# Kernel tuning notes

Measured on AMD Instinct MI355X. Metric: run time of the kernel, lower is better.

The kernel has to match this reference:

```python
import jax, jax.numpy as jnp
import numpy as np

NV, NG, D, K, NB = 4096, 2048, 64, 128, 4
C_IN, C_OUT, E = 128, 8, 32768
SIGMA = 2.5  # rbf sigma used in the non-mp path


def _gcn_conv(x, src, dst, w, b, n):
    # PyG GCNConv (edge_weight=None, self loops already appended to src/dst)
    deg = jax.ops.segment_sum(jnp.ones(src.shape, x.dtype), dst, num_segments=n)
    dinv = jnp.where(deg > 0, 1.0 / jnp.sqrt(deg), 0.0)
    norm = dinv[src] * dinv[dst]
    h = x @ w
    return jax.ops.segment_sum(h[src] * norm[:, None], dst, num_segments=n) + b


def _diff_block(x, mass, evals, evecs, gradX, gradY, t, a_re, a_im, w0, b0, w1, b1, w2, b2):
    # learned-time spectral diffusion
    x_spec = evecs.T @ (x * mass[:, None])                      # [K, D]
    coef = jnp.exp(-evals[:, None] * jnp.clip(t, 1e-8)[None, :])  # [K, D]
    x_diff = evecs @ (coef * x_spec)                            # [NV, D]
    # spatial gradient features: complex grad, learned rotation, tanh of inner product
    gX = gradX @ x_diff                                         # real part  [NV, D]
    gY = gradY @ x_diff                                         # imag part  [NV, D]
    b_re = gX @ a_re - gY @ a_im
    b_im = gY @ a_re + gX @ a_im
    gfeat = jnp.tanh(gX * b_re + gY * b_im)
    f = jnp.concatenate([x, x_diff, gfeat], axis=-1)            # [NV, 3D]
    h = jax.nn.relu(f @ w0 + b0)
    h = jax.nn.relu(h @ w1 + b1)
    return h @ w2 + b2 + x                                      # residual skip


def _forward(surf_x, mass, evals, evecs, gradX, gradY, vertices, graph_x, graph_pos,
             lin1_w, lin1_b, lin2_w, lin2_b, last_w, last_b,
             diff_time, A_re, A_im, mlp_w0, mlp_b0, mlp_w1, mlp_b1, mlp_w2, mlp_b2,
             gcn_w1, gcn_b1, gcn_w2, gcn_b2, edge_index):
    nv, ng = vertices.shape[0], graph_pos.shape[0]
    # dense rbf coupling (torch.no_grad in original -> stop_gradient)
    d2 = (jnp.sum(vertices * vertices, 1)[:, None]
          + jnp.sum(graph_pos * graph_pos, 1)[None, :]
          - 2.0 * (vertices @ graph_pos.T))
    dist = jnp.sqrt(jnp.clip(d2, 0.0))
    rbf = jax.lax.stop_gradient(jnp.exp(-dist / SIGMA))          # [NV, NG]
    diff_x = surf_x @ lin1_w + lin1_b                            # [NV, D]
    gx = graph_x @ lin2_w + lin2_b                               # [NG, D]
    loops = jnp.arange(ng, dtype=edge_index.dtype)
    src = jnp.concatenate([edge_index[0], loops])
    dst = jnp.concatenate([edge_index[1], loops])
    for i in range(NB):
        diff_x = _diff_block(diff_x, mass, evals, evecs, gradX, gradY,
                             diff_time[i], A_re[i], A_im[i],
                             mlp_w0[i], mlp_b0[i], mlp_w1[i], mlp_b1[i], mlp_w2[i], mlp_b2[i])
        gx = rbf.T @ diff_x                                      # surface -> graph
        h = jax.nn.relu(_gcn_conv(gx, src, dst, gcn_w1[i], gcn_b1[i], ng))
        gx = _gcn_conv(h, src, dst, gcn_w2[i], gcn_b2[i], ng)
        diff_x = rbf @ gx                                        # graph -> surface
    return diff_x @ last_w + last_b                              # [NV, C_OUT]


def setup_inputs() -> dict:
    key = jax.random.key(0)
    ks = jax.random.split(key, 24)
    f32 = jnp.float32
    def rn(k, shape, scale=1.0):
        return jax.random.normal(k, shape, f32) * scale
    inp = {
        'surf_x': rn(ks[0], (NV, 5)),
        'mass': jax.random.uniform(ks[1], (NV,), f32, 0.1, 1.0),
        'evals': jnp.sort(jax.random.uniform(ks[2], (K,), f32, 0.0, 50.0)),
        'evecs': rn(ks[3], (NV, K), 1.0 / np.sqrt(NV)),
        'gradX': rn(ks[4], (NV, NV), 1.0 / np.sqrt(NV)),
        'gradY': rn(ks[5], (NV, NV), 1.0 / np.sqrt(NV)),
        'vertices': rn(ks[6], (NV, 3), 5.0),
        'graph_x': rn(ks[7], (NG, C_IN)),
        'graph_pos': rn(ks[8], (NG, 3), 5.0),
        'lin1_w': rn(ks[9], (5, D), 1.0 / np.sqrt(5)),
        'lin1_b': jnp.zeros((D,), f32),
        'lin2_w': rn(ks[10], (C_IN, D), 1.0 / np.sqrt(C_IN)),
        'lin2_b': jnp.zeros((D,), f32),
        'last_w': rn(ks[11], (D, C_OUT), 1.0 / np.sqrt(D)),
        'last_b': jnp.zeros((C_OUT,), f32),
        'diff_time': jax.random.uniform(ks[12], (NB, D), f32, 1e-3, 1.0),
        'A_re': rn(ks[13], (NB, D, D), 1.0 / np.sqrt(D)),
        'A_im': rn(ks[14], (NB, D, D), 1.0 / np.sqrt(D)),
        'mlp_w0': rn(ks[15], (NB, 3 * D, D), 1.0 / np.sqrt(3 * D)),
        'mlp_b0': jnp.zeros((NB, D), f32),
        'mlp_w1': rn(ks[16], (NB, D, D), 1.0 / np.sqrt(D)),
        'mlp_b1': jnp.zeros((NB, D), f32),
        'mlp_w2': rn(ks[17], (NB, D, D), 1.0 / np.sqrt(D)),
        'mlp_b2': jnp.zeros((NB, D), f32),
        'gcn_w1': rn(ks[18], (NB, D, D), 1.0 / np.sqrt(D)),
        'gcn_b1': jnp.zeros((NB, D), f32),
        'gcn_w2': rn(ks[19], (NB, D, D), 1.0 / np.sqrt(D)),
        'gcn_b2': jnp.zeros((NB, D), f32),
        'edge_index': jax.random.randint(ks[20], (2, E), 0, NG, dtype=jnp.int32),
    }
    return inp


def reference(surf_x, mass, evals, evecs, gradX, gradY, vertices, graph_x, graph_pos,
              lin1_w, lin1_b, lin2_w, lin2_b, last_w, last_b,
              diff_time, A_re, A_im, mlp_w0, mlp_b0, mlp_w1, mlp_b1, mlp_w2, mlp_b2,
              gcn_w1, gcn_b1, gcn_w2, gcn_b2, edge_index):
    return _forward(surf_x, mass, evals, evecs, gradX, gradY, vertices, graph_x, graph_pos,
                    lin1_w, lin1_b, lin2_w, lin2_b, last_w, last_b,
                    diff_time, A_re, A_im, mlp_w0, mlp_b0, mlp_w1, mlp_b1, mlp_w2, mlp_b2,
                    gcn_w1, gcn_b1, gcn_w2, gcn_b2, edge_index)
```

## Files before the change

kernel.cpp:

```cpp
#include <hip/hip_runtime.h>
#include <hip/hip_bf16.h>

#define NVV 4096
#define NGG 2048
#define DD 64
#define KSP 128
#define NBLK 4
#define NEDGE 32768
#define COUT 8
#define NSLICE_P 8
#define NSLICE_G 16
#define NSLICE_V 8
#define NSLICE_S 32
#define VS 32

typedef __hip_bfloat16 bf16;
using bf16x8 = __attribute__((ext_vector_type(8))) __bf16;
using s16x8  = __attribute__((ext_vector_type(8))) short;
using f32x4  = __attribute__((ext_vector_type(4))) float;

__device__ __forceinline__ float toF(bf16 x){ return __bfloat162float(x); }
__device__ __forceinline__ float ldin(const void* p, size_t i, int f){
  return f ? toF(((const bf16*)p)[i]) : ((const float*)p)[i];
}
__device__ __forceinline__ short f2bf(float x){
  __bf16 b = (__bf16)x;
  return __builtin_bit_cast(short, b);
}
__device__ __forceinline__ float bf2f(short s){
  return (float)__builtin_bit_cast(__bf16, s);
}
__device__ __forceinline__ bf16x8 ld8(const short* p){
  return __builtin_bit_cast(bf16x8, *(const s16x8*)p);
}
__device__ __forceinline__ void gl16(const short* g, short* l){
  __builtin_amdgcn_global_load_lds((__attribute__((address_space(1))) void*)(g),
                                   (__attribute__((address_space(3))) void*)(l),
                                   16, 0, 0);
}

__global__ void k_probe(const void* __restrict__ mass, int* __restrict__ flag){
  int t = threadIdx.x;
  float v = toF(((const bf16*)mass)[t]);
  bool ok = (v >= 0.05f) && (v <= 1.05f);
  unsigned long long m = __ballot(ok);
  if (t == 0) flag[0] = (m == ~0ull) ? 1 : 0;
}

__global__ void k_csr_zero(int* c){ int g = blockIdx.x*256+threadIdx.x; if (g<NGG) c[g]=0; }
__global__ void k_csr_cnt(const int* __restrict__ ei, int* __restrict__ c){
  int e = blockIdx.x*256+threadIdx.x; if (e<NEDGE) atomicAdd(&c[ei[NEDGE+e]], 1);
}
__global__ void k_csr_scan(const int* __restrict__ cnt, int* __restrict__ off,
                           int* __restrict__ cursor, float* __restrict__ dinv){
  __shared__ int ws[256];
  int t = threadIdx.x;
  int base = t*8;
  int local[8]; int s = 0;
  #pragma unroll
  for (int i=0;i<8;i++){ local[i]=s; s += cnt[base+i]; }
  ws[t] = s;
  __syncthreads();
  for (int o=1;o<256;o<<=1){
    int v = (t>=o) ? ws[t-o] : 0;
    __syncthreads();
    ws[t] += v;
    __syncthreads();
  }
  int pre = (t==0) ? 0 : ws[t-1];
  #pragma unroll
  for (int i=0;i<8;i++){
    int o = pre + local[i];
    off[base+i] = o; cursor[base+i] = o;
    dinv[base+i] = rsqrtf(1.f + (float)cnt[base+i]);
  }
  if (t==255) off[NGG] = pre + s;
}
__global__ void k_csr_fill(const int* __restrict__ ei, int* __restrict__ cursor,
                           int* __restrict__ csrc){
  int e = blockIdx.x*256+threadIdx.x;
  if (e < NEDGE){
    int d = ei[NEDGE+e];
    int p = atomicAdd(&cursor[d], 1);
    csrc[p] = ei[e];
  }
}

__global__ void k_lin1_mx(const void* __restrict__ sx, const void* __restrict__ w,
                          const void* __restrict__ b, const void* __restrict__ mass,
                          float* __restrict__ out, short* __restrict__ btMX,
                          const int* __restrict__ flg){
  const int f = *flg;
  __shared__ short tl[64*68];
  const int t = threadIdx.x;
  const int r = t>>2, c0 = (t&3)*16;
  const size_t v = (size_t)blockIdx.x*64 + r;
  float sxa[5];
  #pragma unroll
  for (int k=0;k<5;k++) sxa[k] = ldin(sx, v*5+k, f);
  const float mv = ldin(mass, v, f);
  float acc[16];
  #pragma unroll
  for (int j=0;j<16;j++){
    float a = ldin(b, c0+j, f);
    #pragma unroll
    for (int k=0;k<5;k++) a += sxa[k]*ldin(w, (size_t)k*DD + c0 + j, f);
    acc[j] = a;
    tl[(size_t)(c0+j)*68 + r] = f2bf(a*mv);
  }
  float* op = out + v*DD + c0;
  ((float4*)op)[0] = *(float4*)&acc[0];
  ((float4*)op)[1] = *(float4*)&acc[4];
  ((float4*)op)[2] = *(float4*)&acc[8];
  ((float4*)op)[3] = *(float4*)&acc[12];
  __syncthreads();
  s16x8 u0, u1;
  #pragma unroll
  for (int j=0;j<8;j++){ u0[j]=tl[(size_t)r*68+c0+j]; u1[j]=tl[(size_t)r*68+c0+8+j]; }
  const int s8 = (r&7)<<3;
  short* dp = btMX + (size_t)blockIdx.x*4096 + (size_t)r*64;
  *(s16x8*)&dp[c0 ^ s8]     = u0;
  *(s16x8*)&dp[(c0+8) ^ s8] = u1;
}

__global__ void k_spec_red(const float* __restrict__ partial, const void* __restrict__ evals,
                           const void* __restrict__ tvec, int boff,
                           short* __restrict__ btA, const int* __restrict__ flg){
  const int f = *flg;
  int idx = blockIdx.x*256 + threadIdx.x;
  int k = idx >> 6, d = idx & 63;
  float sum = 0.f;
  #pragma unroll 8
  for (int s = 0; s < VS; s++) sum += partial[(size_t)s*KSP*DD + idx];
  float t = fmaxf(ldin(tvec, boff + d, f), 1e-8f);
  float val = expf(-ldin(evals, k, f) * t) * sum;
  btA[(size_t)(k>>6)*4096 + (size_t)d*64 + ((k&63) ^ ((d&7)<<3))] = f2bf(val);
}

__global__ void k_cvt_a(const void* __restrict__ src, short* __restrict__ dst,
                        int Kfull, const int* __restrict__ flg){
  const int f = *flg;
  const int t = threadIdx.x;
  const int r = t>>2, c0 = (t&3)*16;
  const size_t row = (size_t)blockIdx.x*64 + r;
  const size_t base = row*(size_t)Kfull + (size_t)blockIdx.y*64 + c0;
  s16x8 v0, v1;
  if (f){
    const short* sp = (const short*)src + base;
    v0 = ((const s16x8*)sp)[0];
    v1 = ((const s16x8*)sp)[1];
  } else {
    const float* sp = (const float*)src + base;
    float tmp[16];
    ((float4*)tmp)[0] = ((const float4*)sp)[0];
    ((float4*)tmp)[1] = ((const float4*)sp)[1];
    ((float4*)tmp)[2] = ((const float4*)sp)[2];
    ((float4*)tmp)[3] = ((const float4*)sp)[3];
    #pragma unroll
    for (int i=0;i<8;i++){ v0[i]=f2bf(tmp[i]); v1[i]=f2bf(tmp[8+i]); }
  }
  const int s8 = (r&7)<<3;
  short* dp = dst + ((size_t)blockIdx.x*(Kfull>>6) + blockIdx.y)*4096 + (size_t)r*64;
  *(s16x8*)&dp[c0 ^ s8]     = v0;
  *(s16x8*)&dp[(c0+8) ^ s8] = v1;
}

__global__ void k_cvt_at(const void* __restrict__ evecs, short* __restrict__ dst,
                         const int* __restrict__ flg){
  const int f = *flg;
  __shared__ short tl[64*68];
  const int t = threadIdx.x;
  const int r = t>>2, c0 = (t&3)*16;
  const int kt = blockIdx.x, s = blockIdx.y;
  const size_t v = (size_t)kt*64 + r;
  #pragma unroll
  for (int j=0;j<16;j++)
    tl[(size_t)(c0+j)*68 + r] = f2bf(ldin(evecs, v*KSP + (size_t)s*64 + c0 + j, f));
  __syncthreads();
  s16x8 u0, u1;
  #pragma unroll
  for (int j=0;j<8;j++){ u0[j]=tl[(size_t)r*68+c0+j]; u1[j]=tl[(size_t)r*68+c0+8+j]; }
  const int s8 = (r&7)<<3;
  short* dp = dst + ((size_t)s*64 + kt)*4096 + (size_t)r*64;
  *(s16x8*)&dp[c0 ^ s8]     = u0;
  *(s16x8*)&dp[(c0+8) ^ s8] = u1;
}

__global__ void k_rbf_pre(const void* __restrict__ P, const void* __restrict__ Q,
                          short* __restrict__ rbfV, short* __restrict__ rbfG,
                          const int* __restrict__ flg){
  const int f = *flg;
  __shared__ short tl[64*68];
  const int t = threadIdx.x;
  const int r = t>>2, c0 = (t&3)*16;
  const int vt = blockIdx.x, gt = blockIdx.y;
  const float px = ldin(P, ((size_t)vt*64+r)*3+0, f);
  const float py = ldin(P, ((size_t)vt*64+r)*3+1, f);
  const float pz = ldin(P, ((size_t)vt*64+r)*3+2, f);
  s16x8 v0, v1;
  #pragma unroll
  for (int j=0;j<16;j++){
    const size_t g = (size_t)gt*64 + c0 + j;
    float dx = px - ldin(Q, g*3+0, f);
    float dy = py - ldin(Q, g*3+1, f);
    float dz = pz - ldin(Q, g*3+2, f);
    short s = f2bf(__expf(-sqrtf(dx*dx+dy*dy+dz*dz)*0.4f));
    if (j<8) v0[j] = s; else v1[j-8] = s;
    tl[(size_t)(c0+j)*68 + r] = s;
  }
  const int s8 = (r&7)<<3;
  short* vp = rbfV + ((size_t)vt*(NGG/64) + gt)*4096 + (size_t)r*64;
  *(s16x8*)&vp[c0 ^ s8]     = v0;
  *(s16x8*)&vp[(c0+8) ^ s8] = v1;
  __syncthreads();
  s16x8 u0, u1;
  #pragma unroll
  for (int j=0;j<8;j++){ u0[j] = tl[(size_t)r*68 + c0 + j]; u1[j] = tl[(size_t)r*68 + c0 + 8 + j]; }
  short* gp = rbfG + ((size_t)gt*(NVV/64) + vt)*4096 + (size_t)r*64;
  *(s16x8*)&gp[c0 ^ s8]     = u0;
  *(s16x8*)&gp[(c0+8) ^ s8] = u1;
}

__global__ void k_cvt_wt(const void* __restrict__ Are, const void* __restrict__ Aim,
                         const void* __restrict__ w0, const void* __restrict__ w1,
                         const void* __restrict__ w2,
                         short* __restrict__ btRe, short* __restrict__ btIm,
                         short* __restrict__ btW0, short* __restrict__ btW1,
                         short* __restrict__ btW2, const int* __restrict__ flg){
  const int f = *flg;
  __shared__ short tl[64*68];
  const int t = threadIdx.x;
  const int r = t>>2, c0 = (t&3)*16;
  const int slot = blockIdx.x, b = blockIdx.y;
  const void* src; size_t soff; short* dst; float scale = 1.f;
  switch(slot){
    case 0: src=Are; soff=(size_t)b*4096; dst=btRe + (size_t)b*2*4096;               break;
    case 1: src=Aim; soff=(size_t)b*4096; dst=btRe + (size_t)b*2*4096 + 4096; scale=-1.f; break;
    case 2: src=Aim; soff=(size_t)b*4096; dst=btIm + (size_t)b*2*4096;               break;
    case 3: src=Are; soff=(size_t)b*4096; dst=btIm + (size_t)b*2*4096 + 4096;        break;
    case 4: case 5: case 6:
      src=w0; soff=(size_t)b*3*4096 + (size_t)(slot-4)*4096;
      dst=btW0 + (size_t)b*3*4096 + (size_t)(slot-4)*4096;                           break;
    case 7: src=w1; soff=(size_t)b*4096; dst=btW1 + (size_t)b*4096;                  break;
    default: src=w2; soff=(size_t)b*4096; dst=btW2 + (size_t)b*4096;                 break;
  }
  #pragma unroll
  for (int j=0;j<16;j++)
    tl[(size_t)(c0+j)*68 + r] = f2bf(scale * ldin(src, soff + (size_t)r*64 + c0 + j, f));
  __syncthreads();
  s16x8 u0, u1;
  #pragma unroll
  for (int j=0;j<8;j++){ u0[j]=tl[(size_t)r*68+c0+j]; u1[j]=tl[(size_t)r*68+c0+8+j]; }
  const int s8 = (r&7)<<3;
  short* dp = dst + (size_t)r*64;
  *(s16x8*)&dp[c0 ^ s8]     = u0;
  *(s16x8*)&dp[(c0+8) ^ s8] = u1;
}

template<int TWO>
__global__ void k_gemm_pre(const short* __restrict__ A0, const short* __restrict__ A1,
                           const short* __restrict__ Bt, float* __restrict__ C,
                           int M, int ktt, int tps, int yoff, short* __restrict__ btOut){
  constexpr int NBUF = TWO ? 3 : 2;
  __shared__ __align__(16) short sm[2*NBUF*4096];
  const int t = threadIdx.x;
  const int w = t>>6, lane = t&63;
  const int fr = lane&15, fq = lane>>4;
  const int strip = blockIdx.x, sl = blockIdx.y;
  const size_t abase = ((size_t)strip*ktt + (size_t)sl*tps)*4096;
  const short* gA0 = A0 + abase;
  const short* gA1 = TWO ? (A1 + abase) : A0;
  const short* gB  = Bt + (size_t)sl*tps*4096;
  const int to = t*8;

  auto stage = [&](int p, int kt){
    short* l = &sm[p*NBUF*4096];
    const size_t ko = (size_t)kt*4096;
    gl16(gA0 + ko + to,        l + (w<<9));
    gl16(gA0 + ko + 2048 + to, l + 2048 + (w<<9));
    if (TWO){
      gl16(gA1 + ko + to,        l + 4096 + (w<<9));
      gl16(gA1 + ko + 2048 + to, l + 6144 + (w<<9));
    }
    short* lb = l + (TWO ? 8192 : 4096);
    gl16(gB + ko + to,        lb + (w<<9));
    gl16(gB + ko + 2048 + to, lb + 2048 + (w<<9));
  };

  f32x4 acc0[4] = {{0,0,0,0},{0,0,0,0},{0,0,0,0},{0,0,0,0}};
  f32x4 acc1[4] = {{0,0,0,0},{0,0,0,0},{0,0,0,0},{0,0,0,0}};

  stage(0, 0);
  int cur = 0;
  const int arow = w*16 + fr;
  const int ax0 = arow*64;
  const int asw = (arow&7)<<3;
  for (int kt=0; kt<tps; ++kt){
    if (kt+1 < tps){
      stage(cur^1, kt+1);
      if constexpr (TWO) asm volatile("s_waitcnt vmcnt(6)" ::: "memory");
      else               asm volatile("s_waitcnt vmcnt(4)" ::: "memory");
    } else {
      asm volatile("s_waitcnt vmcnt(0)" ::: "memory");
    }
    __builtin_amdgcn_s_barrier();
    asm volatile("" ::: "memory");
    const short* As  = &sm[cur*NBUF*4096];
    const short* A1s = As + 4096;
    const short* Bs  = As + (TWO ? 8192 : 4096);
    #pragma unroll
    for (int ks=0; ks<2; ks++){
      const int kx = ks*32 + fq*8;
      bf16x8 a0 = ld8(&As[ax0 + (kx ^ asw)]);
      bf16x8 a1 = TWO ? ld8(&A1s[ax0 + (kx ^ asw)]) : a0;
      #pragma unroll
      for (int nc=0;nc<4;nc++){
        const int brow = nc*16 + fr;
        bf16x8 b = ld8(&Bs[brow*64 + (kx ^ ((brow&7)<<3))]);
        acc0[nc] = __builtin_amdgcn_mfma_f32_16x16x32_bf16(a0, b, acc0[nc], 0, 0, 0);
        if constexpr (TWO)
          acc1[nc] = __builtin_amdgcn_mfma_f32_16x16x32_bf16(a1, b, acc1[nc], 0, 0, 0);
      }
    }
    asm volatile("" ::: "memory");
    __builtin_amdgcn_s_barrier();
    cur ^= 1;
  }
  float* C0 = C + (size_t)sl*M*DD;
  const int row0 = strip*64 + w*16 + fq*4;
  #pragma unroll
  for (int nc=0;nc<4;nc++)
    #pragma unroll
    for (int r=0;r<4;r++)
      C0[(size_t)(row0+r)*DD + nc*16 + fr] = acc0[nc][r];
  if constexpr (TWO){
    float* C1 = C + (size_t)yoff + (size_t)sl*M*DD;
    #pragma unroll
    for (int nc=0;nc<4;nc++)
      #pragma unroll
      for (int r=0;r<4;r++)
        C1[(size_t)(row0+r)*DD + nc*16 + fr] = acc1[nc][r];
  }
  if (btOut){
    #pragma unroll
    for (int nc=0;nc<4;nc++)
      #pragma unroll
      for (int r=0;r<4;r++){
        int k = row0 + r, n = nc*16 + fr;
        btOut[(size_t)(k>>6)*4096 + (size_t)n*64 + ((k&63) ^ ((n&7)<<3))] = f2bf(acc0[nc][r]);
      }
  }
}

__global__ void k_fold_at(const float* __restrict__ part, short* __restrict__ dX,
                          short* __restrict__ dY, int s){
  const int t = threadIdx.x;
  const int r = t>>2, c0 = (t&3)*16;
  const int strip = blockIdx.x;
  float ax[16], ay[16];
  #pragma unroll
  for (int j=0;j<16;j++){ ax[j]=0.f; ay[j]=0.f; }
  const float* pb = part + ((size_t)strip*64 + r)*DD + c0;
  for (int sl=0; sl<NSLICE_P; sl++){
    const float* px = pb + (size_t)sl*NVV*DD;
    const float* py = pb + (size_t)(sl+NSLICE_P)*NVV*DD;
    #pragma unroll
    for (int q=0;q<4;q++){
      float4 a = ((const float4*)px)[q];
      float4 b = ((const float4*)py)[q];
      ax[q*4+0]+=a.x; ax[q*4+1]+=a.y; ax[q*4+2]+=a.z; ax[q*4+3]+=a.w;
      ay[q*4+0]+=b.x; ay[q*4+1]+=b.y; ay[q*4+2]+=b.z; ay[q*4+3]+=b.w;
    }
  }
  s16x8 x0,x1,y0,y1;
  #pragma unroll
  for (int j=0;j<8;j++){ x0[j]=f2bf(ax[j]); x1[j]=f2bf(ax[8+j]);
                         y0[j]=f2bf(ay[j]); y1[j]=f2bf(ay[8+j]); }
  const int s8 = (r&7)<<3;
  short* dpx = dX + ((size_t)strip*2 + s)*4096 + (size_t)r*64;
  short* dpy = dY + ((size_t)strip*2 + s)*4096 + (size_t)r*64;
  *(s16x8*)&dpx[c0 ^ s8]     = x0;
  *(s16x8*)&dpx[(c0+8) ^ s8] = x1;
  *(s16x8*)&dpy[c0 ^ s8]     = y0;
  *(s16x8*)&dpy[(c0+8) ^ s8] = y1;
}

__global__ void k_reduce_mx(const float* __restrict__ P, const void* __restrict__ mass,
                            float* __restrict__ C, short* __restrict__ btMX,
                            int slices, const int* __restrict__ flg){
  const int f = *flg;
  __shared__ short tl[64*68];
  const int t = threadIdx.x;
  const int r = t>>2, c0 = (t&3)*16;
  const size_t v = (size_t)blockIdx.x*64 + r;
  float acc[16];
  #pragma unroll
  for (int j=0;j<16;j++) acc[j] = 0.f;
  const float* pb = P + v*DD + c0;
  for (int s=0;s<slices;s++){
    const float* ps = pb + (size_t)s*NVV*DD;
    #pragma unroll
    for (int q=0;q<4;q++){
      float4 a = ((const float4*)ps)[q];
      acc[q*4+0]+=a.x; acc[q*4+1]+=a.y; acc[q*4+2]+=a.z; acc[q*4+3]+=a.w;
    }
  }
  float* op = C + v*DD + c0;
  ((float4*)op)[0] = *(float4*)&acc[0];
  ((float4*)op)[1] = *(float4*)&acc[4];
  ((float4*)op)[2] = *(float4*)&acc[8];
  ((float4*)op)[3] = *(float4*)&acc[12];
  const float mv = ldin(mass, v, f);
  #pragma unroll
  for (int j=0;j<16;j++) tl[(size_t)(c0+j)*68 + r] = f2bf(acc[j]*mv);
  __syncthreads();
  s16x8 u0, u1;
  #pragma unroll
  for (int j=0;j<8;j++){ u0[j]=tl[(size_t)r*68+c0+j]; u1[j]=tl[(size_t)r*68+c0+8+j]; }
  const int s8 = (r&7)<<3;
  short* dp = btMX + (size_t)blockIdx.x*4096 + (size_t)r*64;
  *(s16x8*)&dp[c0 ^ s8]     = u0;
  *(s16x8*)&dp[(c0+8) ^ s8] = u1;
}

__global__ void k_tail_fused(const short* __restrict__ evsA, const short* __restrict__ GXE,
                             const short* __restrict__ GYE, const short* __restrict__ btA,
                             const float* __restrict__ cur,
                             const short* __restrict__ btRe, const short* __restrict__ btIm,
                             const short* __restrict__ btW0, const short* __restrict__ btW1,
                             const short* __restrict__ btW2,
                             const void* __restrict__ b0, const void* __restrict__ b1,
                             const void* __restrict__ b2, int boff,
                             short* __restrict__ btOut, const int* __restrict__ flg){
  __shared__ __align__(16) short sm[8*4096];
  const int f = *flg;
  const int t = threadIdx.x;
  const int w = t>>6, lane = t&63;
  const int fr = lane&15, fq = lane>>4;
  const int strip = blockIdx.x;
  const int to = t*8;
  const int arow = w*16 + fr;
  const int asw = (arow&7)<<3;
  #pragma unroll
  for (int kt=0; kt<2; kt++){
    const size_t ko = ((size_t)strip*2 + kt)*4096;
    gl16(evsA + ko + to,        &sm[kt*4096] + (w<<9));
    gl16(evsA + ko + 2048 + to, &sm[kt*4096] + 2048 + (w<<9));
    gl16(GXE + ko + to,         &sm[(2+kt)*4096] + (w<<9));
    gl16(GXE + ko + 2048 + to,  &sm[(2+kt)*4096] + 2048 + (w<<9));
    gl16(GYE + ko + to,         &sm[(4+kt)*4096] + (w<<9));
    gl16(GYE + ko + 2048 + to,  &sm[(4+kt)*4096] + 2048 + (w<<9));
    gl16(btA + (size_t)kt*4096 + to,        &sm[(6+kt)*4096] + (w<<9));
    gl16(btA + (size_t)kt*4096 + 2048 + to, &sm[(6+kt)*4096] + 2048 + (w<<9));
  }
  __syncthreads();
  f32x4 aX[4]  = {{0,0,0,0},{0,0,0,0},{0,0,0,0},{0,0,0,0}};
  f32x4 aGX[4] = {{0,0,0,0},{0,0,0,0},{0,0,0,0},{0,0,0,0}};
  f32x4 aGY[4] = {{0,0,0,0},{0,0,0,0},{0,0,0,0},{0,0,0,0}};
  #pragma unroll
  for (int kt=0; kt<2; kt++){
    const short* Ae = &sm[kt*4096];
    const short* Ax = &sm[(2+kt)*4096];
    const short* Ay = &sm[(4+kt)*4096];
    const short* Bs = &sm[(6+kt)*4096];
    #pragma unroll
    for (int ks=0; ks<2; ks++){
      const int kx = ks*32 + fq*8;
      bf16x8 ae = ld8(&Ae[arow*64 + (kx ^ asw)]);
      bf16x8 ax = ld8(&Ax[arow*64 + (kx ^ asw)]);
      bf16x8 ay = ld8(&Ay[arow*64 + (kx ^ asw)]);
      #pragma unroll
      for (int nc=0;nc<4;nc++){
        const int brow = nc*16 + fr;
        bf16x8 b = ld8(&Bs[brow*64 + (kx ^ ((brow&7)<<3))]);
        aX[nc]  = __builtin_amdgcn_mfma_f32_16x16x32_bf16(ae, b, aX[nc], 0, 0, 0);
        aGX[nc] = __builtin_amdgcn_mfma_f32_16x16x32_bf16(ax, b, aGX[nc], 0, 0, 0);
        aGY[nc] = __builtin_amdgcn_mfma_f32_16x16x32_bf16(ay, b, aGY[nc], 0, 0, 0);
      }
    }
  }
  __syncthreads();
  gl16(btRe + to,        &sm[2*4096] + (w<<9));
  gl16(btRe + 2048 + to, &sm[2*4096] + 2048 + (w<<9));
  gl16(btRe + 4096 + to, &sm[3*4096] + (w<<9));
  gl16(btRe + 6144 + to, &sm[3*4096] + 2048 + (w<<9));
  gl16(btIm + to,        &sm[4*4096] + (w<<9));
  gl16(btIm + 2048 + to, &sm[4*4096] + 2048 + (w<<9));
  gl16(btIm + 4096 + to, &sm[5*4096] + (w<<9));
  gl16(btIm + 6144 + to, &sm[5*4096] + 2048 + (w<<9));
  #pragma unroll
  for (int nc=0;nc<4;nc++)
    #pragma unroll
    for (int r2=0;r2<4;r2++){
      const int mi = w*16 + fq*4 + r2, n = nc*16 + fr;
      const int pos = mi*64 + (n ^ ((mi&7)<<3));
      sm[0*4096 + pos] = f2bf(aGX[nc][r2]);
      sm[1*4096 + pos] = f2bf(aGY[nc][r2]);
      sm[7*4096 + pos] = f2bf(aX[nc][r2]);
    }
  {
    const int r = t>>2, c0 = (t&3)*16;
    const float* cp = cur + ((size_t)strip*64 + r)*DD + c0;
    float ca[16];
    ((float4*)ca)[0]=((const float4*)cp)[0]; ((float4*)ca)[1]=((const float4*)cp)[1];
    ((float4*)ca)[2]=((const float4*)cp)[2]; ((float4*)ca)[3]=((const float4*)cp)[3];
    s16x8 v0,v1;
    #pragma unroll
    for (int j=0;j<8;j++){ v0[j]=f2bf(ca[j]); v1[j]=f2bf(ca[8+j]); }
    const int s8 = (r&7)<<3;
    *(s16x8*)&sm[6*4096 + r*64 + (c0 ^ s8)]     = v0;
    *(s16x8*)&sm[6*4096 + r*64 + ((c0+8) ^ s8)] = v1;
  }
  __syncthreads();
  f32x4 re[4] = {{0,0,0,0},{0,0,0,0},{0,0,0,0},{0,0,0,0}};
  f32x4 im[4] = {{0,0,0,0},{0,0,0,0},{0,0,0,0},{0,0,0,0}};
  #pragma unroll
  for (int kt=0; kt<2; kt++){
    const short* As = &sm[kt*4096];
    const short* Br = &sm[(2+kt)*4096];
    const short* Bi = &sm[(4+kt)*4096];
    #pragma unroll
    for (int ks=0; ks<2; ks++){
      const int kx = ks*32 + fq*8;
      bf16x8 a = ld8(&As[arow*64 + (kx ^ asw)]);
      #pragma unroll
      for (int nc=0;nc<4;nc++){
        const int brow = nc*16 + fr, bsw = (brow&7)<<3;
        bf16x8 br_ = ld8(&Br[brow*64 + (kx ^ bsw)]);
        bf16x8 bi_ = ld8(&Bi[brow*64 + (kx ^ bsw)]);
        re[nc] = __builtin_amdgcn_mfma_f32_16x16x32_bf16(a, br_, re[nc], 0, 0, 0);
        im[nc] = __builtin_amdgcn_mfma_f32_16x16x32_bf16(a, bi_, im[nc], 0, 0, 0);
      }
    }
  }
  __syncthreads();
  gl16(btW0 + to,           &sm[2*4096] + (w<<9));
  gl16(btW0 + 2048 + to,    &sm[2*4096] + 2048 + (w<<9));
  gl16(btW0 + 4096 + to,    &sm[3*4096] + (w<<9));
  gl16(btW0 + 6144 + to,    &sm[3*4096] + 2048 + (w<<9));
  gl16(btW0 + 8192 + to,    &sm[4*4096] + (w<<9));
  gl16(btW0 + 10240 + to,   &sm[4*4096] + 2048 + (w<<9));
  gl16(btW1 + to,           &sm[5*4096] + (w<<9));
  gl16(btW1 + 2048 + to,    &sm[5*4096] + 2048 + (w<<9));
  float gfv[4][4];
  #pragma unroll
  for (int nc=0;nc<4;nc++){
    const int n = nc*16 + fr;
    #pragma unroll
    for (int r2=0;r2<4;r2++){
      const int mi = w*16 + fq*4 + r2;
      const int pos = mi*64 + (n ^ ((mi&7)<<3));
      float gx = bf2f(sm[pos]);
      float gy = bf2f(sm[4096 + pos]);
      gfv[nc][r2] = tanhf(gx*re[nc][r2] + gy*im[nc][r2]);
    }
  }
  __syncthreads();
  gl16(btW2 + to,        &sm[1*4096] + (w<<9));
  gl16(btW2 + 2048 + to, &sm[1*4096] + 2048 + (w<<9));
  #pragma unroll
  for (int nc=0;nc<4;nc++)
    #pragma unroll
    for (int r2=0;r2<4;r2++){
      const int mi = w*16 + fq*4 + r2, n = nc*16 + fr;
      sm[mi*64 + (n ^ ((mi&7)<<3))] = f2bf(gfv[nc][r2]);
    }
  __syncthreads();
  f32x4 acc[4] = {{0,0,0,0},{0,0,0,0},{0,0,0,0},{0,0,0,0}};
  #pragma unroll
  for (int kt=0; kt<3; kt++){
    const short* As = &sm[(kt==0 ? 6 : (kt==1 ? 7 : 0))*4096];
    const short* Bs = &sm[(2+kt)*4096];
    #pragma unroll
    for (int ks=0; ks<2; ks++){
      const int kx = ks*32 + fq*8;
      bf16x8 a = ld8(&As[arow*64 + (kx ^ asw)]);
      #pragma unroll
      for (int nc=0;nc<4;nc++){
        const int brow = nc*16 + fr;
        bf16x8 b = ld8(&Bs[brow*64 + (kx ^ ((brow&7)<<3))]);
        acc[nc] = __builtin_amdgcn_mfma_f32_16x16x32_bf16(a, b, acc[nc], 0, 0, 0);
      }
    }
  }
  __syncthreads();
  #pragma unroll
  for (int nc=0;nc<4;nc++){
    float bz = ldin(b0, boff + nc*16 + fr, f);
    #pragma unroll
    for (int r2=0;r2<4;r2++){
      const int mi = w*16 + fq*4 + r2, n = nc*16 + fr;
      sm[6*4096 + mi*64 + (n ^ ((mi&7)<<3))] = f2bf(fmaxf(acc[nc][r2] + bz, 0.f));
    }
  }
  __syncthreads();
  f32x4 a1c[4] = {{0,0,0,0},{0,0,0,0},{0,0,0,0},{0,0,0,0}};
  #pragma unroll
  for (int ks=0; ks<2; ks++){
    const int kx = ks*32 + fq*8;
    bf16x8 a = ld8(&sm[6*4096 + arow*64 + (kx ^ asw)]);
    #pragma unroll
    for (int nc=0;nc<4;nc++){
      const int brow = nc*16 + fr;
      bf16x8 b = ld8(&sm[5*4096 + brow*64 + (kx ^ ((brow&7)<<3))]);
      a1c[nc] = __builtin_amdgcn_mfma_f32_16x16x32_bf16(a, b, a1c[nc], 0, 0, 0);
    }
  }
  #pragma unroll
  for (int nc=0;nc<4;nc++){
    float bz = ldin(b1, boff + nc*16 + fr, f);
    #pragma unroll
    for (int r2=0;r2<4;r2++){
      const int mi = w*16 + fq*4 + r2, n = nc*16 + fr;
      sm[7*4096 + mi*64 + (n ^ ((mi&7)<<3))] = f2bf(fmaxf(a1c[nc][r2] + bz, 0.f));
    }
  }
  __syncthreads();
  f32x4 a2c[4] = {{0,0,0,0},{0,0,0,0},{0,0,0,0},{0,0,0,0}};
  #pragma unroll
  for (int ks=0; ks<2; ks++){
    const int kx = ks*32 + fq*8;
    bf16x8 a = ld8(&sm[7*4096 + arow*64 + (kx ^ asw)]);
    #pragma unroll
    for (int nc=0;nc<4;nc++){
      const int brow = nc*16 + fr;
      bf16x8 b = ld8(&sm[1*4096 + brow*64 + (kx ^ ((brow&7)<<3))]);
      a2c[nc] = __builtin_amdgcn_mfma_f32_16x16x32_bf16(a, b, a2c[nc], 0, 0, 0);
    }
  }
  const int row0 = strip*64 + w*16 + fq*4;
  #pragma unroll
  for (int nc=0;nc<4;nc++){
    float bz = ldin(b2, boff + nc*16 + fr, f);
    #pragma unroll
    for (int r2=0;r2<4;r2++){
      int row = row0 + r2, n = nc*16 + fr;
      float vv = a2c[nc][r2] + bz + cur[(size_t)row*DD + n];
      btOut[(size_t)(row>>6)*4096 + (size_t)n*64 + ((row&63) ^ ((n&7)<<3))] = f2bf(vv);
    }
  }
}

__global__ void k_gcn1(const float* __restrict__ part, const void* __restrict__ W,
                       int woff, const float* __restrict__ dinv,
                       const void* __restrict__ bias, int boff,
                       float* __restrict__ tmp, float* __restrict__ outinit,
                       const int* __restrict__ flg){
  const int f = *flg;
  __shared__ float xs[4][DD];
  int d = threadIdx.x & 63, vl = threadIdx.x >> 6;
  size_t g = (size_t)blockIdx.x*4 + vl;
  float x = 0.f;
  #pragma unroll
  for (int s = 0; s < NSLICE_G; s++) x += part[(size_t)s*NGG*DD + g*DD + d];
  xs[vl][d] = x;
  __syncthreads();
  float acc = 0.f;
  #pragma unroll 8
  for (int k=0;k<DD;k++) acc += xs[vl][k]*ldin(W, (size_t)woff + k*DD + d, f);
  tmp[g*DD+d] = acc;
  float di = dinv[g];
  outinit[g*DD+d] = acc*di*di + ldin(bias, boff + d, f);
}

__global__ void k_gcn2f(const float* __restrict__ selfinit, const float* __restrict__ tmp,
                        const int* __restrict__ off, const int* __restrict__ csrc,
                        const float* __restrict__ dinv, const void* __restrict__ W,
                        int woff, const void* __restrict__ bias, int boff,
                        float* __restrict__ tmp2, float* __restrict__ out2init,
                        const int* __restrict__ flg){
  const int f = *flg;
  __shared__ float xs[4][DD];
  int d = threadIdx.x & 63, vl = threadIdx.x >> 6;
  size_t g = (size_t)blockIdx.x*4 + vl;
  float dg = dinv[g];
  float agg = selfinit[g*DD+d];
  int s1 = off[g+1];
  for (int i = off[g]; i < s1; i++){
    int sv = csrc[i];
    agg += tmp[(size_t)sv*DD+d]*(dinv[sv]*dg);
  }
  xs[vl][d] = fmaxf(agg, 0.f);
  __syncthreads();
  float acc = 0.f;
  #pragma unroll 8
  for (int k=0;k<DD;k++) acc += xs[vl][k]*ldin(W, (size_t)woff + k*DD + d, f);
  tmp2[g*DD+d] = acc;
  out2init[g*DD+d] = acc*dg*dg + ldin(bias, boff + d, f);
}

__global__ void k_aggr_t(const float* __restrict__ selfinit, const float* __restrict__ tmp,
                         const int* __restrict__ off, const int* __restrict__ csrc,
                         const float* __restrict__ dinv, short* __restrict__ dst){
  __shared__ short tl[64*68];
  const int t = threadIdx.x;
  const int r = t>>2, c0 = (t&3)*16;
  const size_t g = (size_t)blockIdx.x*64 + r;
  const float dg = dinv[g];
  float agg[16];
  const float* sp = selfinit + g*DD + c0;
  ((float4*)agg)[0] = ((const float4*)sp)[0];
  ((float4*)agg)[1] = ((const float4*)sp)[1];
  ((float4*)agg)[2] = ((const float4*)sp)[2];
  ((float4*)agg)[3] = ((const float4*)sp)[3];
  const int e1 = off[g+1];
  for (int i = off[g]; i < e1; i++){
    const int sv = csrc[i];
    const float w_ = dinv[sv]*dg;
    const float* tp = tmp + (size_t)sv*DD + c0;
    #pragma unroll
    for (int q=0;q<4;q++){
      float4 a = ((const float4*)tp)[q];
      agg[q*4+0]+=a.x*w_; agg[q*4+1]+=a.y*w_; agg[q*4+2]+=a.z*w_; agg[q*4+3]+=a.w*w_;
    }
  }
  #pragma unroll
  for (int j=0;j<16;j++) tl[(size_t)(c0+j)*68 + r] = f2bf(agg[j]);
  __syncthreads();
  s16x8 u0,u1;
  #pragma unroll
  for (int j=0;j<8;j++){ u0[j]=tl[(size_t)r*68+c0+j]; u1[j]=tl[(size_t)r*68+c0+8+j]; }
  const int s8 = (r&7)<<3;
  short* dp = dst + (size_t)blockIdx.x*4096 + (size_t)r*64;
  *(s16x8*)&dp[c0 ^ s8]     = u0;
  *(s16x8*)&dp[(c0+8) ^ s8] = u1;
}

__global__ void k_final(const float* __restrict__ x, const void* __restrict__ w,
                        const void* __restrict__ b, void* __restrict__ outv,
                        const int* __restrict__ flg){
  const int f = *flg;
  int idx = blockIdx.x*256 + threadIdx.x;
  int v = idx >> 3, c = idx & 7;
  float acc = ldin(b, c, f);
  #pragma unroll 8
  for (int k=0;k<DD;k++) acc += x[(size_t)v*DD+k]*ldin(w, (size_t)k*COUT+c, f);
  if (f) ((bf16*)outv)[idx] = __float2bfloat16(acc);
  else   ((float*)outv)[idx] = acc;
}

extern "C" void kernel_launch(void* const* d_in, const int* in_sizes, int n_in,
                              void* d_out, int out_size, void* d_ws, size_t ws_size,
                              hipStream_t stream){
  (void)in_sizes; (void)n_in;
  const void* surf_x   = d_in[0];
  const void* mass     = d_in[1];
  const void* evals    = d_in[2];
  const void* evecs    = d_in[3];
  const void* gradX    = d_in[4];
  const void* gradY    = d_in[5];
  const void* vertices = d_in[6];
  const void* gpos     = d_in[8];
  const void* lin1_w   = d_in[9];
  const void* lin1_b   = d_in[10];
  const void* last_w   = d_in[13];
  const void* last_b   = d_in[14];
  const void* dtime    = d_in[15];
  const void* A_re     = d_in[16];
  const void* A_im     = d_in[17];
  const void* mw0      = d_in[18];
  const void* mb0      = d_in[19];
  const void* mw1      = d_in[20];
  const void* mb1      = d_in[21];
  const void* mw2      = d_in[22];
  const void* mb2      = d_in[23];
  const void* gw1      = d_in[24];
  const void* gb1      = d_in[25];
  const void* gw2      = d_in[26];
  const void* gb2      = d_in[27];
  const int*  ei       = (const int*)d_in[28];

  const size_t REQUIRED = (size_t)126*1024*1024;
  if (ws_size < REQUIRED){
    hipMemsetAsync(d_out, 0, (size_t)out_size*2, stream);
    return;
  }
  char* p = (char*)d_ws;
  auto alloc = [&](size_t bytes)->void*{
    void* r = (void*)p;
    p += (bytes + 255) & ~(size_t)255;
    return r;
  };
  float* part  = (float*)alloc((size_t)16*NVV*DD*4);
  float* bufA  = (float*)alloc((size_t)NVV*DD*4);
  float* tmpg  = (float*)alloc((size_t)NGG*DD*4);
  float* hg    = (float*)alloc((size_t)NGG*DD*4);
  float* tmp2  = (float*)alloc((size_t)NGG*DD*4);
  float* o2    = (float*)alloc((size_t)NGG*DD*4);
  float* dinv  = (float*)alloc((size_t)NGG*4);
  int*   flg   = (int*)alloc(256);
  int*   cnt   = (int*)alloc((size_t)NGG*4);
  int*   off   = (int*)alloc((size_t)(NGG+1)*4);
  int*   curs  = (int*)alloc((size_t)NGG*4);
  int*   csrc  = (int*)alloc((size_t)NEDGE*4);
  short* gXs   = (short*)alloc((size_t)NVV*NVV*2);
  short* gYs   = (short*)alloc((size_t)NVV*NVV*2);
  short* rbfV  = (short*)alloc((size_t)NVV*NGG*2);
  short* rbfG  = (short*)alloc((size_t)NVV*NGG*2);
  short* evsT  = (short*)alloc((size_t)NVV*KSP*2);
  short* evs   = (short*)alloc((size_t)NVV*KSP*2);
  short* GXE   = (short*)alloc((size_t)NVV*KSP*2);
  short* GYE   = (short*)alloc((size_t)NVV*KSP*2);
  short* btA   = (short*)alloc((size_t)KSP*DD*2);
  short* btB   = (short*)alloc((size_t)NVV*DD*2);
  short* btMX  = (short*)alloc((size_t)NVV*DD*2);
  short* btRe  = (short*)alloc((size_t)NBLK*2*4096*2);
  short* btIm  = (short*)alloc((size_t)NBLK*2*4096*2);
  short* btW0  = (short*)alloc((size_t)NBLK*3*4096*2);
  short* btW1  = (short*)alloc((size_t)NBLK*4096*2);
  short* btW2  = (short*)alloc((size_t)NBLK*4096*2);

  k_probe<<<1, 64, 0, stream>>>(mass, flg);
  k_csr_zero<<<NGG/256, 256, 0, stream>>>(cnt);
  k_csr_cnt <<<NEDGE/256, 256, 0, stream>>>(ei, cnt);
  k_csr_scan<<<1, 256, 0, stream>>>(cnt, off, curs, dinv);
  k_csr_fill<<<NEDGE/256, 256, 0, stream>>>(ei, curs, csrc);
  k_lin1_mx <<<NVV/64, 256, 0, stream>>>(surf_x, lin1_w, lin1_b, mass, bufA, btMX, flg);
  k_cvt_a<<<dim3(NVV/64, NVV/64), 256, 0, stream>>>(gradX, gXs, NVV, flg);
  k_cvt_a<<<dim3(NVV/64, NVV/64), 256, 0, stream>>>(gradY, gYs, NVV, flg);
  k_cvt_a<<<dim3(NVV/64, KSP/64), 256, 0, stream>>>(evecs, evs, KSP, flg);
  k_cvt_at<<<dim3(NVV/64, KSP/64), 256, 0, stream>>>(evecs, evsT, flg);
  k_rbf_pre<<<dim3(NVV/64, NGG/64), 256, 0, stream>>>(vertices, gpos, rbfV, rbfG, flg);
  k_cvt_wt<<<dim3(9, NBLK), 256, 0, stream>>>(A_re, A_im, mw0, mw1, mw2,
                                              btRe, btIm, btW0, btW1, btW2, flg);
  for (int s = 0; s < 2; s++){
    k_gemm_pre<1><<<dim3(NVV/64, NSLICE_P), 256, 0, stream>>>(
        gXs, gYs, evsT + (size_t)s*64*4096, part,
        NVV, NVV/64, (NVV/64)/NSLICE_P, NSLICE_P*NVV*DD, nullptr);
    k_fold_at<<<NVV/64, 256, 0, stream>>>(part, GXE, GYE, s);
  }

  float* cur = bufA;
  for (int b = 0; b < NBLK; b++){
    k_gemm_pre<0><<<dim3(KSP/64, NSLICE_S), 256, 0, stream>>>(evsT, evsT, btMX, part,
        KSP, NVV/64, (NVV/64)/NSLICE_S, 0, nullptr);
    k_spec_red<<<KSP*DD/256, 256, 0, stream>>>(part, evals, dtime, b*DD, btA, flg);
    k_tail_fused<<<NVV/64, 256, 0, stream>>>(evs, GXE, GYE, btA, cur,
        btRe + (size_t)b*2*4096, btIm + (size_t)b*2*4096,
        btW0 + (size_t)b*3*4096, btW1 + (size_t)b*4096, btW2 + (size_t)b*4096,
        mb0, mb1, mb2, b*DD, btB, flg);
    k_gemm_pre<0><<<dim3(NGG/64, NSLICE_G), 256, 0, stream>>>(rbfG, rbfG, btB, part,
        NGG, NVV/64, (NVV/64)/NSLICE_G, 0, nullptr);
    k_gcn1<<<NGG/4, 256, 0, stream>>>(part, gw1, b*DD*DD, dinv, gb1, b*DD, tmpg, hg, flg);
    k_gcn2f<<<NGG/4, 256, 0, stream>>>(hg, tmpg, off, csrc, dinv, gw2, b*DD*DD,
                                       gb2, b*DD, tmp2, o2, flg);
    k_aggr_t<<<NGG/64, 256, 0, stream>>>(o2, tmp2, off, csrc, dinv, btB);
    k_gemm_pre<0><<<dim3(NVV/64, NSLICE_V), 256, 0, stream>>>(rbfV, rbfV, btB, part,
        NVV, NGG/64, (NGG/64)/NSLICE_V, 0, nullptr);
    k_reduce_mx<<<NVV/64, 256, 0, stream>>>(part, mass, cur, btMX, NSLICE_V, flg);
  }
  k_final<<<NVV*COUT/256, 256, 0, stream>>>(cur, last_w, last_b, d_out, flg);
}
```

Measured before the change: 618.8 us.

## Fuse gradX/gradY bf16 conversion into a single GXE/GYE precompute GEMM

```diff
diff --git a/kernel.cpp b/kernel.cpp
--- a/kernel.cpp
+++ b/kernel.cpp
@@ -8,7 +8,6 @@
 #define NBLK 4
 #define NEDGE 32768
 #define COUT 8
-#define NSLICE_P 8
 #define NSLICE_G 16
 #define NSLICE_V 8
 #define NSLICE_S 32
@@ -352,18 +351,101 @@
   }
 }
 
+__global__ void k_gxe_raw(const void* __restrict__ gradX, const void* __restrict__ gradY,
+                          const short* __restrict__ evsT, float* __restrict__ part,
+                          const int* __restrict__ flg){
+  const int f = *flg;
+  __shared__ __align__(16) short sm[4*4096];
+  const int t = threadIdx.x;
+  const int w = t>>6, lane = t&63;
+  const int fr = lane&15, fq = lane>>4;
+  const int strip = blockIdx.x, ksl = blockIdx.y;
+  const int sr = t>>2, sc = (t&3)*16;
+  const int to = t*8;
+  const int arow = w*16 + fr;
+  const int asw = (arow&7)<<3;
+  const int s8 = (sr&7)<<3;
+  f32x4 aX0[4] = {{0,0,0,0},{0,0,0,0},{0,0,0,0},{0,0,0,0}};
+  f32x4 aX1[4] = {{0,0,0,0},{0,0,0,0},{0,0,0,0},{0,0,0,0}};
+  f32x4 aY0[4] = {{0,0,0,0},{0,0,0,0},{0,0,0,0},{0,0,0,0}};
+  f32x4 aY1[4] = {{0,0,0,0},{0,0,0,0},{0,0,0,0},{0,0,0,0}};
+  for (int kt=0; kt<8; ++kt){
+    const int ktg = ksl*8 + kt;
+    const size_t abase = ((size_t)strip*64 + sr)*NVV + (size_t)ktg*64 + sc;
+    s16x8 x0, x1, y0, y1;
+    if (f==0){
+      const float* ax = (const float*)gradX + abase;
+      const float* ay = (const float*)gradY + abase;
+      float bx[16], by[16];
+      ((float4*)bx)[0]=((const float4*)ax)[0]; ((float4*)bx)[1]=((const float4*)ax)[1];
+      ((float4*)bx)[2]=((const float4*)ax)[2]; ((float4*)bx)[3]=((const float4*)ax)[3];
+      ((float4*)by)[0]=((const float4*)ay)[0]; ((float4*)by)[1]=((const float4*)ay)[1];
+      ((float4*)by)[2]=((const float4*)ay)[2]; ((float4*)by)[3]=((const float4*)ay)[3];
+      #pragma unroll
+      for (int j=0;j<8;j++){ x0[j]=f2bf(bx[j]); x1[j]=f2bf(bx[8+j]);
+                             y0[j]=f2bf(by[j]); y1[j]=f2bf(by[8+j]); }
+    } else {
+      const short* ax = (const short*)gradX + abase;
+      const short* ay = (const short*)gradY + abase;
+      x0 = ((const s16x8*)ax)[0]; x1 = ((const s16x8*)ax)[1];
+      y0 = ((const s16x8*)ay)[0]; y1 = ((const s16x8*)ay)[1];
+    }
+    *(s16x8*)&sm[0*4096 + sr*64 + (sc ^ s8)]     = x0;
+    *(s16x8*)&sm[0*4096 + sr*64 + ((sc+8) ^ s8)] = x1;
+    *(s16x8*)&sm[1*4096 + sr*64 + (sc ^ s8)]     = y0;
+    *(s16x8*)&sm[1*4096 + sr*64 + ((sc+8) ^ s8)] = y1;
+    gl16(evsT + (size_t)ktg*4096 + to,             &sm[2*4096] + (w<<9));
+    gl16(evsT + (size_t)ktg*4096 + 2048 + to,      &sm[2*4096] + 2048 + (w<<9));
+    gl16(evsT + (size_t)(64+ktg)*4096 + to,        &sm[3*4096] + (w<<9));
+    gl16(evsT + (size_t)(64+ktg)*4096 + 2048 + to, &sm[3*4096] + 2048 + (w<<9));
+    __syncthreads();
+    #pragma unroll
+    for (int ks=0; ks<2; ks++){
+      const int kx = ks*32 + fq*8;
+      bf16x8 aXv = ld8(&sm[0*4096 + arow*64 + (kx ^ asw)]);
+      bf16x8 aYv = ld8(&sm[1*4096 + arow*64 + (kx ^ asw)]);
+      #pragma unroll
+      for (int nc=0;nc<4;nc++){
+        const int brow = nc*16 + fr, bsw = (brow&7)<<3;
+        bf16x8 b0 = ld8(&sm[2*4096 + brow*64 + (kx ^ bsw)]);
+        bf16x8 b1 = ld8(&sm[3*4096 + brow*64 + (kx ^ bsw)]);
+        aX0[nc] = __builtin_amdgcn_mfma_f32_16x16x32_bf16(aXv, b0, aX0[nc], 0, 0, 0);
+        aX1[nc] = __builtin_amdgcn_mfma_f32_16x16x32_bf16(aXv, b1, aX1[nc], 0, 0, 0);
+        aY0[nc] = __builtin_amdgcn_mfma_f32_16x16x32_bf16(aYv, b0, aY0[nc], 0, 0, 0);
+        aY1[nc] = __builtin_amdgcn_mfma_f32_16x16x32_bf16(aYv, b1, aY1[nc], 0, 0, 0);
+      }
+    }
+    __syncthreads();
+  }
+  const int row0 = strip*64 + w*16 + fq*4;
+  float* C0 = part + (size_t)(ksl)*NVV*DD;
+  float* C1 = part + (size_t)(8+ksl)*NVV*DD;
+  float* C2 = part + (size_t)(16+ksl)*NVV*DD;
+  float* C3 = part + (size_t)(24+ksl)*NVV*DD;
+  #pragma unroll
+  for (int nc=0;nc<4;nc++)
+    #pragma unroll
+    for (int r=0;r<4;r++){
+      const size_t o = (size_t)(row0+r)*DD + nc*16 + fr;
+      C0[o] = aX0[nc][r];
+      C1[o] = aX1[nc][r];
+      C2[o] = aY0[nc][r];
+      C3[o] = aY1[nc][r];
+    }
+}
+
 __global__ void k_fold_at(const float* __restrict__ part, short* __restrict__ dX,
-                          short* __restrict__ dY, int s){
+                          short* __restrict__ dY){
   const int t = threadIdx.x;
   const int r = t>>2, c0 = (t&3)*16;
-  const int strip = blockIdx.x;
+  const int strip = blockIdx.x, s = blockIdx.y;
   float ax[16], ay[16];
   #pragma unroll
   for (int j=0;j<16;j++){ ax[j]=0.f; ay[j]=0.f; }
   const float* pb = part + ((size_t)strip*64 + r)*DD + c0;
-  for (int sl=0; sl<NSLICE_P; sl++){
-    const float* px = pb + (size_t)sl*NVV*DD;
-    const float* py = pb + (size_t)(sl+NSLICE_P)*NVV*DD;
+  for (int sl=0; sl<8; sl++){
+    const float* px = pb + (size_t)(s*8+sl)*NVV*DD;
+    const float* py = pb + (size_t)(16+s*8+sl)*NVV*DD;
     #pragma unroll
     for (int q=0;q<4;q++){
       float4 a = ((const float4*)px)[q];
@@ -770,7 +852,7 @@
   const void* gb2      = d_in[27];
   const int*  ei       = (const int*)d_in[28];
 
-  const size_t REQUIRED = (size_t)126*1024*1024;
+  const size_t REQUIRED = (size_t)100*1024*1024;
   if (ws_size < REQUIRED){
     hipMemsetAsync(d_out, 0, (size_t)out_size*2, stream);
     return;
@@ -781,7 +863,7 @@
     p += (bytes + 255) & ~(size_t)255;
     return r;
   };
-  float* part  = (float*)alloc((size_t)16*NVV*DD*4);
+  float* part  = (float*)alloc((size_t)32*NVV*DD*4);
   float* bufA  = (float*)alloc((size_t)NVV*DD*4);
   float* tmpg  = (float*)alloc((size_t)NGG*DD*4);
   float* hg    = (float*)alloc((size_t)NGG*DD*4);
@@ -793,8 +875,6 @@
   int*   off   = (int*)alloc((size_t)(NGG+1)*4);
   int*   curs  = (int*)alloc((size_t)NGG*4);
   int*   csrc  = (int*)alloc((size_t)NEDGE*4);
-  short* gXs   = (short*)alloc((size_t)NVV*NVV*2);
-  short* gYs   = (short*)alloc((size_t)NVV*NVV*2);
   short* rbfV  = (short*)alloc((size_t)NVV*NGG*2);
   short* rbfG  = (short*)alloc((size_t)NVV*NGG*2);
   short* evsT  = (short*)alloc((size_t)NVV*KSP*2);
@@ -816,19 +896,13 @@
   k_csr_scan<<<1, 256, 0, stream>>>(cnt, off, curs, dinv);
   k_csr_fill<<<NEDGE/256, 256, 0, stream>>>(ei, curs, csrc);
   k_lin1_mx <<<NVV/64, 256, 0, stream>>>(surf_x, lin1_w, lin1_b, mass, bufA, btMX, flg);
-  k_cvt_a<<<dim3(NVV/64, NVV/64), 256, 0, stream>>>(gradX, gXs, NVV, flg);
-  k_cvt_a<<<dim3(NVV/64, NVV/64), 256, 0, stream>>>(gradY, gYs, NVV, flg);
   k_cvt_a<<<dim3(NVV/64, KSP/64), 256, 0, stream>>>(evecs, evs, KSP, flg);
   k_cvt_at<<<dim3(NVV/64, KSP/64), 256, 0, stream>>>(evecs, evsT, flg);
   k_rbf_pre<<<dim3(NVV/64, NGG/64), 256, 0, stream>>>(vertices, gpos, rbfV, rbfG, flg);
   k_cvt_wt<<<dim3(9, NBLK), 256, 0, stream>>>(A_re, A_im, mw0, mw1, mw2,
                                               btRe, btIm, btW0, btW1, btW2, flg);
-  for (int s = 0; s < 2; s++){
-    k_gemm_pre<1><<<dim3(NVV/64, NSLICE_P), 256, 0, stream>>>(
-        gXs, gYs, evsT + (size_t)s*64*4096, part,
-        NVV, NVV/64, (NVV/64)/NSLICE_P, NSLICE_P*NVV*DD, nullptr);
-    k_fold_at<<<NVV/64, 256, 0, stream>>>(part, GXE, GYE, s);
-  }
+  k_gxe_raw<<<dim3(NVV/64, 8), 256, 0, stream>>>(gradX, gradY, evsT, part, flg);
+  k_fold_at<<<dim3(NVV/64, 2), 256, 0, stream>>>(part, GXE, GYE);
 
   float* cur = bufA;
   for (int b = 0; b < NBLK; b++){
```

Measured after the change: 584.9 us. -5.5%, faster.
